# Optimization experiments

Hardware: AMD Instinct MI355X
Metric: run time of the kernel (lower is better)

## Reference

```python
import jax, jax.numpy as jnp
import numpy as np

KP_THRESHOLD = 20.0
KP_BETA = 0.5
TARGET_ENTROPY = 6.0
LOG2 = 0.6931471805599453

B, C, H, W = 8, 18, 256, 256
N_HYP, K = 1024, 9


def setup_inputs() -> dict:
    key = jax.random.key(0)
    ks = jax.random.split(key, 16)
    inp = {}
    for i, sfx in enumerate(['_L', '_R']):
        o = 8 * i
        inp['vertex_pred' + sfx] = jax.random.normal(ks[o + 0], (B, C, H, W), jnp.float32)
        inp['vertex_gt' + sfx] = jax.random.normal(ks[o + 1], (B, C, H, W), jnp.float32)
        inp['mask' + sfx] = jax.random.randint(ks[o + 2], (B, H, W), 0, 2, jnp.int32)
        inp['seg' + sfx] = jax.random.normal(ks[o + 3], (B, 2, H, W), jnp.float32)
        inp['keypoints' + sfx] = jax.random.normal(ks[o + 4], (B, N_HYP, K, 2), jnp.float32) * 10.0
        inp['scores' + sfx] = jax.random.normal(ks[o + 5], (B, N_HYP, K), jnp.float32)
        inp['kpt_2d' + sfx] = jax.random.normal(ks[o + 6], (B, K, 2), jnp.float32) * 10.0
        inp['offset' + sfx] = jax.random.normal(ks[o + 7], (B, 2), jnp.float32)
    inp['softmax_a'] = jnp.asarray(0.5, jnp.float32)
    inp['epoch'] = 100
    return inp


def _smooth_l1_sum(x, y):
    d = jnp.abs(x - y)
    return jnp.sum(jnp.where(d < 1.0, 0.5 * d * d, d - 0.5))


def _side_losses(vertex_pred, vertex_gt, mask, seg, keypoints, scores, kpt_2d, a):
    w = mask[:, None].astype(jnp.float32)                      # [B,1,H,W]
    vote = _smooth_l1_sum(vertex_pred * w, vertex_gt * w)
    ws = jnp.sum(w)
    vote = jnp.where(ws > 0, vote / jnp.maximum(ws, 1.0) / vertex_gt.shape[1], vote)
    # CrossEntropyLoss (mean over B*H*W pixels)
    logp = jax.nn.log_softmax(seg, axis=1)                     # [B,2,H,W]
    nll = -jnp.take_along_axis(logp, mask[:, None], axis=1)[:, 0]
    seg_loss = jnp.mean(nll)
    # DSAC expected keypoint loss: softmax over hypothesis axis
    probs = jax.nn.softmax(a * scores, axis=1)                 # [B,N,K]
    dist = jnp.linalg.norm(keypoints - kpt_2d[:, None], axis=-1)
    kp_loss = jnp.mean(jnp.sum(probs * dist, axis=1))
    # entropy loss on detached scores (entropy in bits)
    s = jax.lax.stop_gradient(a * scores)
    p = jax.nn.softmax(s, axis=1)
    lp = jax.nn.log_softmax(s, axis=1) / LOG2
    entropy = jnp.mean(-jnp.sum(p * lp, axis=1), axis=1)       # [B]
    ent_loss = jnp.sum(jnp.abs(entropy - TARGET_ENTROPY)) / scores.shape[0]
    return vote, seg_loss, kp_loss, ent_loss


def _epipolar(kp_L, off_L, sc_L, kp_R, off_R, sc_R, a):
    # keypoints detached; add per-image crop offsets -> global coords
    kp_L = jax.lax.stop_gradient(kp_L) + off_L[:, None, None, :]
    kp_R = jax.lax.stop_gradient(kp_R) + off_R[:, None, None, :]
    kL, kR = jax.random.split(jax.random.key(1234))
    idx_L = jax.random.categorical(kL, jax.lax.stop_gradient(a * sc_L), axis=1)  # [B,K]
    idx_R = jax.random.categorical(kR, jax.lax.stop_gradient(a * sc_R), axis=1)
    yL = jnp.take_along_axis(kp_L[..., 1], idx_L[:, None, :], axis=1)[:, 0]      # [B,K]
    yR = jnp.take_along_axis(kp_R[..., 1], idx_R[:, None, :], axis=1)[:, 0]
    d = jnp.abs(yL - yR)  # sqrt((yL-yR)^2)
    d = jnp.where(jnp.isfinite(d), d, 0.0)
    return jnp.mean(d)    # mean over K then over B == global mean


def reference(vertex_pred_L, vertex_gt_L, mask_L, seg_L, keypoints_L, scores_L, kpt_2d_L, offset_L,
              vertex_pred_R, vertex_gt_R, mask_R, seg_R, keypoints_R, scores_R, kpt_2d_R, offset_R,
              softmax_a, epoch):
    vL, sL, kL, eL = _side_losses(vertex_pred_L, vertex_gt_L, mask_L, seg_L, keypoints_L, scores_L, kpt_2d_L, softmax_a)
    vR, sR, kR, eR = _side_losses(vertex_pred_R, vertex_gt_R, mask_R, seg_R, keypoints_R, scores_R, kpt_2d_R, softmax_a)
    vote_loss = (vL + vR) * 0.5
    seg_loss = (sL + sR) * 0.5
    kp_loss = (kL + kR) * 0.5
    entropy_loss = (eL + eR) * 0.5
    kp_w = jax.nn.sigmoid(KP_BETA * (KP_THRESHOLD - jax.lax.stop_gradient(kp_loss)))
    vote_w = 1.0 - kp_w
    if epoch > 49:
        epi = _epipolar(keypoints_L, offset_L, scores_L, keypoints_R, offset_R, scores_R, softmax_a)
        vertex_loss = kp_w * (kp_loss + epi) + vote_w * vote_loss
    else:
        vertex_loss = kp_w * kp_loss + vote_w * vote_loss
    loss = vertex_loss + entropy_loss + seg_loss
    return loss
```

## Files before the change

### kernel.cpp

```cpp
#include <hip/hip_runtime.h>
#include <stdint.h>
#include <math.h>

#define HWPIX 65536
#define NCH   18
#define NHYP  1024
#define NK    9
#define NBK   72
#define NPIXBLK 512
#define INV_LOG2 1.4426950408889634f
#define TINYF 1.1754943508222875e-38f

#define OFS_VOTE 64
#define OFS_CNT  (OFS_VOTE + 2 * NPIXBLK)
#define OFS_SEG  (OFS_CNT  + 2 * NPIXBLK)
#define OFS_KP   (OFS_SEG  + 2 * NPIXBLK)
#define OFS_ENT  (OFS_KP   + 2 * NBK)
#define OFS_Y    (OFS_ENT  + 2 * NBK)

__host__ __device__ inline void tf2x32(uint32_t k0, uint32_t k1,
                                       uint32_t x0, uint32_t x1,
                                       uint32_t& o0, uint32_t& o1) {
  uint32_t ks2 = k0 ^ k1 ^ 0x1BD11BDAu;
  x0 += k0; x1 += k1;
#define TFR(r) { x0 += x1; x1 = (x1 << (r)) | (x1 >> (32 - (r))); x1 ^= x0; }
  TFR(13) TFR(15) TFR(26) TFR(6)   x0 += k1;  x1 += ks2 + 1u;
  TFR(17) TFR(29) TFR(16) TFR(24)  x0 += ks2; x1 += k0 + 2u;
  TFR(13) TFR(15) TFR(26) TFR(6)   x0 += k0;  x1 += k1 + 3u;
  TFR(17) TFR(29) TFR(16) TFR(24)  x0 += k1;  x1 += ks2 + 4u;
  TFR(13) TFR(15) TFR(26) TFR(6)   x0 += ks2; x1 += k0 + 5u;
#undef TFR
  o0 = x0; o1 = x1;
}

__device__ inline float blk_sum(float v, float* sm) {
  int t = threadIdx.x;
  sm[t] = v; __syncthreads();
  for (int off = 128; off > 0; off >>= 1) {
    if (t < off) sm[t] += sm[t + off];
    __syncthreads();
  }
  float r = sm[0]; __syncthreads();
  return r;
}

__device__ inline float nll2(float s0, float s1, int lbl) {
  float mx = fmaxf(s0, s1);
  float l = mx + logf(expf(s0 - mx) + expf(s1 - mx));
  return l - (lbl ? s1 : s0);
}

__global__ __launch_bounds__(256) void pixel_kernel(
    const float* __restrict__ vpL, const float* __restrict__ vgL,
    const int*   __restrict__ mkL, const float* __restrict__ sgL,
    const float* __restrict__ vpR, const float* __restrict__ vgR,
    const int*   __restrict__ mkR, const float* __restrict__ sgR,
    float* __restrict__ ws) {
  const int side = blockIdx.y;
  const float* vp = side ? vpR : vpL;
  const float* vg = side ? vgR : vgL;
  const int*   mk = side ? mkR : mkL;
  const float* sg = side ? sgR : sgL;

  const int g  = blockIdx.x * 256 + threadIdx.x;
  const int p0 = g * 4;
  const int b  = p0 >> 16;
  const int hw = p0 & (HWPIX - 1);

  const int4 m4 = *(const int4*)(mk + p0);
  const float w0 = (float)m4.x, w1 = (float)m4.y, w2 = (float)m4.z, w3 = (float)m4.w;

  float vote = 0.f;
  const size_t vbase = (size_t)b * (NCH * HWPIX) + hw;
#pragma unroll
  for (int c = 0; c < NCH; ++c) {
    const float4 p = *(const float4*)(vp + vbase + (size_t)c * HWPIX);
    const float4 q = *(const float4*)(vg + vbase + (size_t)c * HWPIX);
    float dd;
    dd = fabsf(p.x - q.x) * w0; vote += (dd < 1.f) ? 0.5f * dd * dd : dd - 0.5f;
    dd = fabsf(p.y - q.y) * w1; vote += (dd < 1.f) ? 0.5f * dd * dd : dd - 0.5f;
    dd = fabsf(p.z - q.z) * w2; vote += (dd < 1.f) ? 0.5f * dd * dd : dd - 0.5f;
    dd = fabsf(p.w - q.w) * w3; vote += (dd < 1.f) ? 0.5f * dd * dd : dd - 0.5f;
  }
  const float cnt = w0 + w1 + w2 + w3;

  const size_t sbase = (size_t)b * (2 * HWPIX) + hw;
  const float4 s0 = *(const float4*)(sg + sbase);
  const float4 s1 = *(const float4*)(sg + sbase + HWPIX);
  float seg = 0.f;
  seg += nll2(s0.x, s1.x, m4.x);
  seg += nll2(s0.y, s1.y, m4.y);
  seg += nll2(s0.z, s1.z, m4.z);
  seg += nll2(s0.w, s1.w, m4.w);

  __shared__ float sm[256];
  float v  = blk_sum(vote, sm);
  float c2 = blk_sum(cnt, sm);
  float sg2 = blk_sum(seg, sm);
  if (threadIdx.x == 0) {
    ws[OFS_VOTE + side * NPIXBLK + blockIdx.x] = v;
    ws[OFS_CNT  + side * NPIXBLK + blockIdx.x] = c2;
    ws[OFS_SEG  + side * NPIXBLK + blockIdx.x] = sg2;
  }
}

__global__ __launch_bounds__(256) void hyp_kernel(
    const float* __restrict__ scL, const float* __restrict__ kpL,
    const float* __restrict__ k2L, const float* __restrict__ ofL,
    const float* __restrict__ scR, const float* __restrict__ kpR,
    const float* __restrict__ k2R, const float* __restrict__ ofR,
    const float* __restrict__ aPtr,
    uint32_t kLa, uint32_t kLb, uint32_t kRa, uint32_t kRb,
    float* __restrict__ ws) {
  const int side = blockIdx.y;
  const float* sc = side ? scR : scL;
  const float* kp = side ? kpR : kpL;
  const float* k2 = side ? k2R : k2L;
  const float* of = side ? ofR : ofL;
  const uint32_t K0 = side ? kRa : kLa;
  const uint32_t K1 = side ? kRb : kLb;
  const int bk = blockIdx.x;
  const int b = bk / NK, k = bk % NK;
  const int t = threadIdx.x;
  const float a = aPtr[0];
  const float kx = k2[(b * NK + k) * 2 + 0];
  const float ky = k2[(b * NK + k) * 2 + 1];
  const float2* kp2 = (const float2*)kp;

  float s[4], d[4], gv[4];
#pragma unroll
  for (int j = 0; j < 4; ++j) {
    const int n = t + j * 256;
    const size_t idx = ((size_t)b * NHYP + n) * NK + k;
    s[j] = a * sc[idx];
    const float2 xy = kp2[idx];
    const float dx = xy.x - kx, dy = xy.y - ky;
    d[j] = sqrtf(dx * dx + dy * dy);
    uint32_t o0, o1;
    tf2x32(K0, K1, 0u, (uint32_t)idx, o0, o1);
    const uint32_t bits = o0 ^ o1;
    float u = __uint_as_float((bits >> 9) | 0x3F800000u) - 1.0f;
    u = fmaxf(TINYF, u * (1.0f - TINYF) + TINYF);
    gv[j] = -logf(-logf(u)) + s[j];
  }

  __shared__ float sm[256];
  __shared__ int   si[256];

  float mx = fmaxf(fmaxf(s[0], s[1]), fmaxf(s[2], s[3]));
  sm[t] = mx; __syncthreads();
  for (int off = 128; off > 0; off >>= 1) {
    if (t < off) sm[t] = fmaxf(sm[t], sm[t + off]);
    __syncthreads();
  }
  mx = sm[0]; __syncthreads();

  float Z = 0.f, Sd = 0.f, Ss = 0.f;
#pragma unroll
  for (int j = 0; j < 4; ++j) {
    const float e = expf(s[j] - mx);
    Z  += e;
    Sd += e * d[j];
    Ss += e * (s[j] - mx);
  }
  Z  = blk_sum(Z, sm);
  Sd = blk_sum(Sd, sm);
  Ss = blk_sum(Ss, sm);

  float bv = gv[0]; int bi = t;
#pragma unroll
  for (int j = 1; j < 4; ++j) {
    const int n = t + j * 256;
    if (gv[j] > bv) { bv = gv[j]; bi = n; }
  }
  sm[t] = bv; si[t] = bi; __syncthreads();
  for (int off = 128; off > 0; off >>= 1) {
    if (t < off) {
      const float v2 = sm[t + off]; const int i2 = si[t + off];
      if (v2 > sm[t] || (v2 == sm[t] && i2 < si[t])) { sm[t] = v2; si[t] = i2; }
    }
    __syncthreads();
  }

  if (t == 0) {
    ws[OFS_KP  + side * NBK + bk] = Sd / Z;
    ws[OFS_ENT + side * NBK + bk] = (logf(Z) - Ss / Z) * INV_LOG2;
    const int n = si[0];
    ws[OFS_Y + side * NBK + bk] =
        kp2[((size_t)b * NHYP + n) * NK + k].y + of[b * 2 + 1];
  }
}

__global__ __launch_bounds__(256) void final_kernel(
    const int* __restrict__ epochPtr, const float* __restrict__ ws,
    float* __restrict__ out) {
  __shared__ float sm[256];
  const int t = threadIdx.x;
  float voteS[2], cntS[2], segS[2], kpS[2], entS[2];
  for (int side = 0; side < 2; ++side) {
    float a;
    a = 0.f; for (int j = t; j < NPIXBLK; j += 256) a += ws[OFS_VOTE + side * NPIXBLK + j];
    voteS[side] = blk_sum(a, sm);
    a = 0.f; for (int j = t; j < NPIXBLK; j += 256) a += ws[OFS_CNT + side * NPIXBLK + j];
    cntS[side] = blk_sum(a, sm);
    a = 0.f; for (int j = t; j < NPIXBLK; j += 256) a += ws[OFS_SEG + side * NPIXBLK + j];
    segS[side] = blk_sum(a, sm);
    a = (t < NBK) ? ws[OFS_KP + side * NBK + t] : 0.f;
    kpS[side] = blk_sum(a, sm);
    a = 0.f;
    if (t < 8) {
      float es = 0.f;
      for (int k = 0; k < NK; ++k) es += ws[OFS_ENT + side * NBK + t * NK + k];
      a = fabsf(es / (float)NK - 6.0f);
    }
    entS[side] = blk_sum(a, sm);
  }
  float e = 0.f;
  if (t < NBK) {
    const float dy = fabsf(ws[OFS_Y + t] - ws[OFS_Y + NBK + t]);
    e = isfinite(dy) ? dy : 0.f;
  }
  const float epiSum = blk_sum(e, sm);

  if (t == 0) {
    const float voteL = (cntS[0] > 0.f) ? voteS[0] / fmaxf(cntS[0], 1.f) / (float)NCH : voteS[0];
    const float voteR = (cntS[1] > 0.f) ? voteS[1] / fmaxf(cntS[1], 1.f) / (float)NCH : voteS[1];
    const float segL = segS[0] / 524288.f;
    const float segR = segS[1] / 524288.f;
    const float kpLm = kpS[0] / (float)NBK, kpRm = kpS[1] / (float)NBK;
    const float entL = entS[0] / 8.f, entR = entS[1] / 8.f;

    const float vote_loss = 0.5f * (voteL + voteR);
    const float seg_loss  = 0.5f * (segL + segR);
    const float kp_loss   = 0.5f * (kpLm + kpRm);
    const float ent_loss  = 0.5f * (entL + entR);
    const float kp_w  = 1.f / (1.f + expf(-0.5f * (20.f - kp_loss)));
    const float vote_w = 1.f - kp_w;
    float vertex;
    if (epochPtr[0] > 49) {
      const float epi = epiSum / (float)NBK;
      vertex = kp_w * (kp_loss + epi) + vote_w * vote_loss;
    } else {
      vertex = kp_w * kp_loss + vote_w * vote_loss;
    }
    out[0] = vertex + ent_loss + seg_loss;
  }
}

extern "C" void kernel_launch(void* const* d_in, const int* in_sizes, int n_in,
                              void* d_out, int out_size, void* d_ws, size_t ws_size,
                              hipStream_t stream) {
  (void)in_sizes; (void)n_in; (void)out_size; (void)ws_size;
  const float* vpL = (const float*)d_in[0];
  const float* vgL = (const float*)d_in[1];
  const int*   mkL = (const int*)  d_in[2];
  const float* sgL = (const float*)d_in[3];
  const float* kpL = (const float*)d_in[4];
  const float* scL = (const float*)d_in[5];
  const float* k2L = (const float*)d_in[6];
  const float* ofL = (const float*)d_in[7];
  const float* vpR = (const float*)d_in[8];
  const float* vgR = (const float*)d_in[9];
  const int*   mkR = (const int*)  d_in[10];
  const float* sgR = (const float*)d_in[11];
  const float* kpR = (const float*)d_in[12];
  const float* scR = (const float*)d_in[13];
  const float* k2R = (const float*)d_in[14];
  const float* ofR = (const float*)d_in[15];
  const float* aP  = (const float*)d_in[16];
  const int*   epP = (const int*)  d_in[17];
  float* ws  = (float*)d_ws;
  float* out = (float*)d_out;

  uint32_t kLa, kLb, kRa, kRb;
  tf2x32(0u, 1234u, 0u, 0u, kLa, kLb);
  tf2x32(0u, 1234u, 0u, 1u, kRa, kRb);

  pixel_kernel<<<dim3(NPIXBLK, 2), 256, 0, stream>>>(
      vpL, vgL, mkL, sgL, vpR, vgR, mkR, sgR, ws);
  hyp_kernel<<<dim3(NBK, 2), 256, 0, stream>>>(
      scL, kpL, k2L, ofL, scR, kpR, k2R, ofR, aP, kLa, kLb, kRa, kRb, ws);
  final_kernel<<<1, 256, 0, stream>>>(epP, ws, out);
}
```

Baseline: 53.37 us.

## Split pixel kernel channels across grid groups to raise memory parallelism

The pixel kernel now launches six channel groups per pixel block (3 channels each) along a new grid dimension. Each block issues all its loads up front and writes a per-group vote partial sum. The mask count and segmentation loss are computed only in group 0, and the final kernel reduces six times as many vote partials. This aims to put more blocks and outstanding loads in flight on the bandwidth-bound pixel pass, at the cost of rereading the mask per group and more partials to reduce. The segmentation NLL also uses one exp instead of two.

Result: slower. 55.75 us (+4.5%).

```diff
diff --git a/kernel.cpp b/kernel.cpp
--- a/kernel.cpp
+++ b/kernel.cpp
@@ -8,11 +8,13 @@
 #define NK    9
 #define NBK   72
 #define NPIXBLK 512
+#define NGRP  6
+#define CPG   3
 #define INV_LOG2 1.4426950408889634f
 #define TINYF 1.1754943508222875e-38f
 
 #define OFS_VOTE 64
-#define OFS_CNT  (OFS_VOTE + 2 * NPIXBLK)
+#define OFS_CNT  (OFS_VOTE + 2 * NGRP * NPIXBLK)
 #define OFS_SEG  (OFS_CNT  + 2 * NPIXBLK)
 #define OFS_KP   (OFS_SEG  + 2 * NPIXBLK)
 #define OFS_ENT  (OFS_KP   + 2 * NBK)
@@ -45,8 +47,9 @@
 }
 
 __device__ inline float nll2(float s0, float s1, int lbl) {
-  float mx = fmaxf(s0, s1);
-  float l = mx + logf(expf(s0 - mx) + expf(s1 - mx));
+  const float mx = fmaxf(s0, s1);
+  const float mn = fminf(s0, s1);
+  const float l = mx + logf(1.0f + expf(mn - mx));
   return l - (lbl ? s1 : s0);
 }
 
@@ -56,7 +59,8 @@
     const float* __restrict__ vpR, const float* __restrict__ vgR,
     const int*   __restrict__ mkR, const float* __restrict__ sgR,
     float* __restrict__ ws) {
-  const int side = blockIdx.y;
+  const int side = blockIdx.z;
+  const int grp  = blockIdx.y;
   const float* vp = side ? vpR : vpL;
   const float* vg = side ? vgR : vgL;
   const int*   mk = side ? mkR : mkL;
@@ -70,37 +74,44 @@
   const int4 m4 = *(const int4*)(mk + p0);
   const float w0 = (float)m4.x, w1 = (float)m4.y, w2 = (float)m4.z, w3 = (float)m4.w;
 
+  float4 p[CPG], q[CPG];
+  const size_t vbase = (size_t)b * (NCH * HWPIX) + (size_t)(grp * CPG) * HWPIX + hw;
+#pragma unroll
+  for (int c = 0; c < CPG; ++c) p[c] = *(const float4*)(vp + vbase + (size_t)c * HWPIX);
+#pragma unroll
+  for (int c = 0; c < CPG; ++c) q[c] = *(const float4*)(vg + vbase + (size_t)c * HWPIX);
+
   float vote = 0.f;
-  const size_t vbase = (size_t)b * (NCH * HWPIX) + hw;
-#pragma unroll
-  for (int c = 0; c < NCH; ++c) {
-    const float4 p = *(const float4*)(vp + vbase + (size_t)c * HWPIX);
-    const float4 q = *(const float4*)(vg + vbase + (size_t)c * HWPIX);
+#pragma unroll
+  for (int c = 0; c < CPG; ++c) {
     float dd;
-    dd = fabsf(p.x - q.x) * w0; vote += (dd < 1.f) ? 0.5f * dd * dd : dd - 0.5f;
-    dd = fabsf(p.y - q.y) * w1; vote += (dd < 1.f) ? 0.5f * dd * dd : dd - 0.5f;
-    dd = fabsf(p.z - q.z) * w2; vote += (dd < 1.f) ? 0.5f * dd * dd : dd - 0.5f;
-    dd = fabsf(p.w - q.w) * w3; vote += (dd < 1.f) ? 0.5f * dd * dd : dd - 0.5f;
-  }
-  const float cnt = w0 + w1 + w2 + w3;
-
-  const size_t sbase = (size_t)b * (2 * HWPIX) + hw;
-  const float4 s0 = *(const float4*)(sg + sbase);
-  const float4 s1 = *(const float4*)(sg + sbase + HWPIX);
-  float seg = 0.f;
-  seg += nll2(s0.x, s1.x, m4.x);
-  seg += nll2(s0.y, s1.y, m4.y);
-  seg += nll2(s0.z, s1.z, m4.z);
-  seg += nll2(s0.w, s1.w, m4.w);
+    dd = fabsf(p[c].x - q[c].x) * w0; vote += (dd < 1.f) ? 0.5f * dd * dd : dd - 0.5f;
+    dd = fabsf(p[c].y - q[c].y) * w1; vote += (dd < 1.f) ? 0.5f * dd * dd : dd - 0.5f;
+    dd = fabsf(p[c].z - q[c].z) * w2; vote += (dd < 1.f) ? 0.5f * dd * dd : dd - 0.5f;
+    dd = fabsf(p[c].w - q[c].w) * w3; vote += (dd < 1.f) ? 0.5f * dd * dd : dd - 0.5f;
+  }
 
   __shared__ float sm[256];
-  float v  = blk_sum(vote, sm);
-  float c2 = blk_sum(cnt, sm);
-  float sg2 = blk_sum(seg, sm);
-  if (threadIdx.x == 0) {
-    ws[OFS_VOTE + side * NPIXBLK + blockIdx.x] = v;
-    ws[OFS_CNT  + side * NPIXBLK + blockIdx.x] = c2;
-    ws[OFS_SEG  + side * NPIXBLK + blockIdx.x] = sg2;
+  const float v = blk_sum(vote, sm);
+  if (threadIdx.x == 0)
+    ws[OFS_VOTE + (side * NGRP + grp) * NPIXBLK + blockIdx.x] = v;
+
+  if (grp == 0) {
+    const float cnt = w0 + w1 + w2 + w3;
+    const size_t sbase = (size_t)b * (2 * HWPIX) + hw;
+    const float4 s0 = *(const float4*)(sg + sbase);
+    const float4 s1 = *(const float4*)(sg + sbase + HWPIX);
+    float seg = 0.f;
+    seg += nll2(s0.x, s1.x, m4.x);
+    seg += nll2(s0.y, s1.y, m4.y);
+    seg += nll2(s0.z, s1.z, m4.z);
+    seg += nll2(s0.w, s1.w, m4.w);
+    const float c2 = blk_sum(cnt, sm);
+    const float sg2 = blk_sum(seg, sm);
+    if (threadIdx.x == 0) {
+      ws[OFS_CNT + side * NPIXBLK + blockIdx.x] = c2;
+      ws[OFS_SEG + side * NPIXBLK + blockIdx.x] = sg2;
+    }
   }
 }
 
@@ -199,7 +210,9 @@
   float voteS[2], cntS[2], segS[2], kpS[2], entS[2];
   for (int side = 0; side < 2; ++side) {
     float a;
-    a = 0.f; for (int j = t; j < NPIXBLK; j += 256) a += ws[OFS_VOTE + side * NPIXBLK + j];
+    a = 0.f;
+    for (int j = t; j < NGRP * NPIXBLK; j += 256)
+      a += ws[OFS_VOTE + side * NGRP * NPIXBLK + j];
     voteS[side] = blk_sum(a, sm);
     a = 0.f; for (int j = t; j < NPIXBLK; j += 256) a += ws[OFS_CNT + side * NPIXBLK + j];
     cntS[side] = blk_sum(a, sm);
@@ -276,7 +289,7 @@
   tf2x32(0u, 1234u, 0u, 0u, kLa, kLb);
   tf2x32(0u, 1234u, 0u, 1u, kRa, kRb);
 
-  pixel_kernel<<<dim3(NPIXBLK, 2), 256, 0, stream>>>(
+  pixel_kernel<<<dim3(NPIXBLK, NGRP, 2), 256, 0, stream>>>(
       vpL, vgL, mkL, sgL, vpR, vgR, mkR, sgR, ws);
   hyp_kernel<<<dim3(NBK, 2), 256, 0, stream>>>(
       scL, kpL, k2L, ofL, scR, kpR, k2R, ofR, aP, kLa, kLb, kRa, kRb, ws);
```

## Split pixel kernel channels across two block halves with explicit load prefetch

Applied to the files above, without the earlier changes.

The pixel kernel now launches twice as many blocks, each handling nine of the eighteen vertex channels for its pixels, so more blocks and memory requests are in flight on a bandwidth-bound pass. Channel loads are double-buffered by hand and the launch bounds request higher occupancy. Only the first half-block computes the segmentation loss and mask count, and the workspace layout and final reduction are resized to match. The log-sum-exp for two classes is simplified to use a single exp. The cost is reloading the mask in both halves and some imbalance between the halves' work.

Measured after the change: 52.49 us. Within noise of the previous version (-1.6%).

```diff
diff --git a/kernel.cpp b/kernel.cpp
--- a/kernel.cpp
+++ b/kernel.cpp
@@ -7,14 +7,16 @@
 #define NHYP  1024
 #define NK    9
 #define NBK   72
-#define NPIXBLK 512
 #define INV_LOG2 1.4426950408889634f
 #define TINYF 1.1754943508222875e-38f
 
+#define NVB_SIDE 1024
+#define NSB_SIDE 512
+
 #define OFS_VOTE 64
-#define OFS_CNT  (OFS_VOTE + 2 * NPIXBLK)
-#define OFS_SEG  (OFS_CNT  + 2 * NPIXBLK)
-#define OFS_KP   (OFS_SEG  + 2 * NPIXBLK)
+#define OFS_CNT  (OFS_VOTE + 2 * NVB_SIDE)
+#define OFS_SEG  (OFS_CNT  + 2 * NSB_SIDE)
+#define OFS_KP   (OFS_SEG  + 2 * NSB_SIDE)
 #define OFS_ENT  (OFS_KP   + 2 * NBK)
 #define OFS_Y    (OFS_ENT  + 2 * NBK)
 
@@ -44,63 +46,92 @@
   return r;
 }
 
+__device__ inline float sl1(float x, float y, float w) {
+  const float dd = fabsf(x - y) * w;
+  return (dd < 1.f) ? 0.5f * dd * dd : dd - 0.5f;
+}
+
 __device__ inline float nll2(float s0, float s1, int lbl) {
-  float mx = fmaxf(s0, s1);
-  float l = mx + logf(expf(s0 - mx) + expf(s1 - mx));
+  const float mx = fmaxf(s0, s1);
+  const float mn = fminf(s0, s1);
+  const float l = mx + logf(1.0f + expf(mn - mx));
   return l - (lbl ? s1 : s0);
 }
 
-__global__ __launch_bounds__(256) void pixel_kernel(
+#define LD4(p) (*(const float4*)(p))
+
+__global__ __launch_bounds__(256, 8) void pixel_kernel(
     const float* __restrict__ vpL, const float* __restrict__ vgL,
     const int*   __restrict__ mkL, const float* __restrict__ sgL,
     const float* __restrict__ vpR, const float* __restrict__ vgR,
     const int*   __restrict__ mkR, const float* __restrict__ sgR,
     float* __restrict__ ws) {
-  const int side = blockIdx.y;
+  const int t     = threadIdx.x;
+  const int bid   = blockIdx.x;
+  const int side  = bid >> 10;
+  const int v     = bid & 1023;
+  const int b     = v >> 7;
+  const int half  = (v >> 6) & 1;
+  const int blk64 = v & 63;
+  const int hwq   = blk64 * 256 + t;
+
   const float* vp = side ? vpR : vpL;
   const float* vg = side ? vgR : vgL;
   const int*   mk = side ? mkR : mkL;
   const float* sg = side ? sgR : sgL;
 
-  const int g  = blockIdx.x * 256 + threadIdx.x;
-  const int p0 = g * 4;
-  const int b  = p0 >> 16;
-  const int hw = p0 & (HWPIX - 1);
-
-  const int4 m4 = *(const int4*)(mk + p0);
+  const int4 m4 = *(const int4*)(mk + ((size_t)b << 16) + ((size_t)hwq << 2));
   const float w0 = (float)m4.x, w1 = (float)m4.y, w2 = (float)m4.z, w3 = (float)m4.w;
 
-  float vote = 0.f;
-  const size_t vbase = (size_t)b * (NCH * HWPIX) + hw;
+  float4 s0 = make_float4(0.f, 0.f, 0.f, 0.f), s1 = s0;
+  if (half == 0) {
+    const size_t soff = ((size_t)b << 17) + ((size_t)hwq << 2);
+    s0 = LD4(sg + soff);
+    s1 = LD4(sg + soff + HWPIX);
+  }
+
+  const size_t pbase = ((size_t)(b * NCH + half * 9) << 16) + ((size_t)hwq << 2);
+  const float* pp = vp + pbase;
+  const float* qq = vg + pbase;
+
+  float4 Pa = LD4(pp);              float4 Qa = LD4(qq);
+  float4 Pb = LD4(pp + HWPIX);      float4 Qb = LD4(qq + HWPIX);
+
+  float acc = 0.f;
 #pragma unroll
-  for (int c = 0; c < NCH; ++c) {
-    const float4 p = *(const float4*)(vp + vbase + (size_t)c * HWPIX);
-    const float4 q = *(const float4*)(vg + vbase + (size_t)c * HWPIX);
-    float dd;
-    dd = fabsf(p.x - q.x) * w0; vote += (dd < 1.f) ? 0.5f * dd * dd : dd - 0.5f;
-    dd = fabsf(p.y - q.y) * w1; vote += (dd < 1.f) ? 0.5f * dd * dd : dd - 0.5f;
-    dd = fabsf(p.z - q.z) * w2; vote += (dd < 1.f) ? 0.5f * dd * dd : dd - 0.5f;
-    dd = fabsf(p.w - q.w) * w3; vote += (dd < 1.f) ? 0.5f * dd * dd : dd - 0.5f;
-  }
-  const float cnt = w0 + w1 + w2 + w3;
-
-  const size_t sbase = (size_t)b * (2 * HWPIX) + hw;
-  const float4 s0 = *(const float4*)(sg + sbase);
-  const float4 s1 = *(const float4*)(sg + sbase + HWPIX);
-  float seg = 0.f;
-  seg += nll2(s0.x, s1.x, m4.x);
-  seg += nll2(s0.y, s1.y, m4.y);
-  seg += nll2(s0.z, s1.z, m4.z);
-  seg += nll2(s0.w, s1.w, m4.w);
+  for (int j = 0; j < 9; ++j) {
+    float4 pc, qc;
+    if ((j & 1) == 0) {
+      pc = Pa; qc = Qa;
+      if (j + 2 < 9) { Pa = LD4(pp + (size_t)(j + 2) * HWPIX); Qa = LD4(qq + (size_t)(j + 2) * HWPIX); }
+    } else {
+      pc = Pb; qc = Qb;
+      if (j + 2 < 9) { Pb = LD4(pp + (size_t)(j + 2) * HWPIX); Qb = LD4(qq + (size_t)(j + 2) * HWPIX); }
+    }
+    acc += sl1(pc.x, qc.x, w0);
+    acc += sl1(pc.y, qc.y, w1);
+    acc += sl1(pc.z, qc.z, w2);
+    acc += sl1(pc.w, qc.w, w3);
+  }
 
   __shared__ float sm[256];
-  float v  = blk_sum(vote, sm);
-  float c2 = blk_sum(cnt, sm);
-  float sg2 = blk_sum(seg, sm);
-  if (threadIdx.x == 0) {
-    ws[OFS_VOTE + side * NPIXBLK + blockIdx.x] = v;
-    ws[OFS_CNT  + side * NPIXBLK + blockIdx.x] = c2;
-    ws[OFS_SEG  + side * NPIXBLK + blockIdx.x] = sg2;
+  const float rvote = blk_sum(acc, sm);
+  if (t == 0) ws[OFS_VOTE + side * NVB_SIDE + v] = rvote;
+
+  if (half == 0) {
+    float seg = 0.f;
+    seg += nll2(s0.x, s1.x, m4.x);
+    seg += nll2(s0.y, s1.y, m4.y);
+    seg += nll2(s0.z, s1.z, m4.z);
+    seg += nll2(s0.w, s1.w, m4.w);
+    const float cnt = w0 + w1 + w2 + w3;
+    const float rcnt = blk_sum(cnt, sm);
+    const float rseg = blk_sum(seg, sm);
+    if (t == 0) {
+      const int s = b * 64 + blk64;
+      ws[OFS_CNT + side * NSB_SIDE + s] = rcnt;
+      ws[OFS_SEG + side * NSB_SIDE + s] = rseg;
+    }
   }
 }
 
@@ -199,11 +230,11 @@
   float voteS[2], cntS[2], segS[2], kpS[2], entS[2];
   for (int side = 0; side < 2; ++side) {
     float a;
-    a = 0.f; for (int j = t; j < NPIXBLK; j += 256) a += ws[OFS_VOTE + side * NPIXBLK + j];
+    a = 0.f; for (int j = t; j < NVB_SIDE; j += 256) a += ws[OFS_VOTE + side * NVB_SIDE + j];
     voteS[side] = blk_sum(a, sm);
-    a = 0.f; for (int j = t; j < NPIXBLK; j += 256) a += ws[OFS_CNT + side * NPIXBLK + j];
+    a = 0.f; for (int j = t; j < NSB_SIDE; j += 256) a += ws[OFS_CNT + side * NSB_SIDE + j];
     cntS[side] = blk_sum(a, sm);
-    a = 0.f; for (int j = t; j < NPIXBLK; j += 256) a += ws[OFS_SEG + side * NPIXBLK + j];
+    a = 0.f; for (int j = t; j < NSB_SIDE; j += 256) a += ws[OFS_SEG + side * NSB_SIDE + j];
     segS[side] = blk_sum(a, sm);
     a = (t < NBK) ? ws[OFS_KP + side * NBK + t] : 0.f;
     kpS[side] = blk_sum(a, sm);
@@ -276,8 +307,7 @@
   tf2x32(0u, 1234u, 0u, 0u, kLa, kLb);
   tf2x32(0u, 1234u, 0u, 1u, kRa, kRb);
 
-  pixel_kernel<<<dim3(NPIXBLK, 2), 256, 0, stream>>>(
-      vpL, vgL, mkL, sgL, vpR, vgR, mkR, sgR, ws);
+  pixel_kernel<<<2048, 256, 0, stream>>>(vpL, vgL, mkL, sgL, vpR, vgR, mkR, sgR, ws);
   hyp_kernel<<<dim3(NBK, 2), 256, 0, stream>>>(
       scL, kpL, k2L, ofL, scR, kpR, k2R, ofR, aP, kLa, kLb, kRa, kRb, ws);
   final_kernel<<<1, 256, 0, stream>>>(epP, ws, out);
```
